# Kernel optimization log

Hardware: AMD Instinct MI355X
Metric: run time of the kernel (lower is better)

## Reference

```python
import jax, jax.numpy as jnp
import numpy as np

N_NODES = 10000
N_EDGES = 160000
F_IN, D, N_CLS = 300, 1024, 10
NEG_SLOPE = 0.2


def setup_inputs() -> dict:
    key = jax.random.key(0)
    ks = jax.random.split(key, 12)
    s = 0.05  # small init scale for numerical sanity
    return {
        "x": jax.random.normal(ks[0], (N_NODES, F_IN), jnp.float32),
        "edge_index": jax.random.randint(ks[1], (2, N_EDGES), 0, N_NODES, jnp.int64),
        "W1": jax.random.normal(ks[2], (F_IN, D), jnp.float32) * s,
        "att_src1": jax.random.normal(ks[3], (D,), jnp.float32) * s,
        "att_dst1": jax.random.normal(ks[4], (D,), jnp.float32) * s,
        "b1": jnp.zeros((D,), jnp.float32),
        "W2": jax.random.normal(ks[5], (D, D), jnp.float32) * s,
        "att_src2": jax.random.normal(ks[6], (D,), jnp.float32) * s,
        "att_dst2": jax.random.normal(ks[7], (D,), jnp.float32) * s,
        "b2": jnp.zeros((D,), jnp.float32),
        "fc_w": jax.random.normal(ks[8], (D, N_CLS), jnp.float32) * s,
        "fc_b": jnp.zeros((N_CLS,), jnp.float32),
    }


def gat_conv(x, src, dst, W, a_src, a_dst, b):
    # PyG GATConv, heads=1: h = x W; e_ij = leaky_relu(a_src.h_j + a_dst.h_i)
    h = x @ W                      # [N, D]
    e = jax.nn.leaky_relu((h @ a_src)[src] + (h @ a_dst)[dst], NEG_SLOPE)  # [E]
    # scatter-softmax over edges grouped by destination node
    m = jax.lax.stop_gradient(jax.ops.segment_max(e, dst, num_segments=N_NODES))
    ex = jnp.exp(e - m[dst])
    denom = jax.ops.segment_sum(ex, dst, num_segments=N_NODES)
    alpha = ex / denom[dst]        # [E]
    out = jax.ops.segment_sum(alpha[:, None] * h[src], dst, num_segments=N_NODES)
    return out + b


def reference(x, edge_index, W1, att_src1, att_dst1, b1,
              W2, att_src2, att_dst2, b2, fc_w, fc_b):
    loops = jnp.arange(N_NODES, dtype=edge_index.dtype)
    src = jnp.concatenate([edge_index[0], loops])  # add_self_loops=True
    dst = jnp.concatenate([edge_index[1], loops])
    emb = jax.nn.relu(gat_conv(x, src, dst, W1, att_src1, att_dst1, b1))
    emb = jax.nn.relu(gat_conv(emb, src, dst, W2, att_src2, att_dst2, b2))
    return jax.nn.softmax(emb @ fc_w + fc_b, axis=-1)
```

## Files before the change

kernel.cpp:

```cpp
#include <hip/hip_runtime.h>
#include <hip/hip_bf16.h>
#include <hip/hip_fp16.h>
#include <math.h>

#define N_NODES 10000
#define N_EDGES 160000
#define E_TOT   (N_EDGES + N_NODES)
#define F_IN    300
#define D       1024
#define N_CLS   10
#define NEG_SLOPE 0.2f

#define MP      10112
#define KP1     320
#define KP2     1024

typedef __attribute__((ext_vector_type(8))) _Float16 f16x8;
typedef __attribute__((ext_vector_type(4))) float f32x4;

#define GLOAD_LDS16(g, l) __builtin_amdgcn_global_load_lds( \
    (const __attribute__((address_space(1))) void*)(g), \
    (__attribute__((address_space(3))) void*)(l), 16, 0, 0)


__global__ void init_deg(int* __restrict__ deg) {
    int i = blockIdx.x * blockDim.x + threadIdx.x;
    if (i < N_NODES) deg[i] = 1;
}

__global__ void count_edges(const int* __restrict__ dst, int* __restrict__ deg) {
    int e = blockIdx.x * blockDim.x + threadIdx.x;
    if (e < N_EDGES) atomicAdd(&deg[dst[e]], 1);
}

__global__ void scan_offs(const int* __restrict__ deg, int* __restrict__ offs,
                          int* __restrict__ pos) {
    __shared__ int sbuf[1024];
    __shared__ int scarry;
    int t = threadIdx.x;
    if (t == 0) { scarry = 0; offs[0] = 0; }
    __syncthreads();
    for (int base = 0; base < N_NODES; base += 1024) {
        int v = (base + t < N_NODES) ? deg[base + t] : 0;
        sbuf[t] = v;
        __syncthreads();
        for (int off = 1; off < 1024; off <<= 1) {
            int add = (t >= off) ? sbuf[t - off] : 0;
            __syncthreads();
            sbuf[t] += add;
            __syncthreads();
        }
        int carry = scarry;
        if (base + t < N_NODES) {
            int incl = carry + sbuf[t];
            offs[base + t + 1] = incl;
            pos[base + t]      = incl - v;
        }
        __syncthreads();
        if (t == 1023) scarry = carry + sbuf[1023];
        __syncthreads();
    }
}

__global__ void scatter_edges(const int* __restrict__ src, const int* __restrict__ dst,
                              int* __restrict__ pos, int* __restrict__ ssrc) {
    int e = blockIdx.x * blockDim.x + threadIdx.x;
    if (e < N_EDGES) {
        int d = dst[e];
        int p = atomicAdd(&pos[d], 1);
        ssrc[p] = src[e];
    } else if (e < E_TOT) {
        int i = e - N_EDGES;
        int p = atomicAdd(&pos[i], 1);
        ssrc[p] = i;
    }
}


__global__ void prep_uv(const float* __restrict__ W1, const float* __restrict__ as1,
                        const float* __restrict__ ad1, const float* __restrict__ W2,
                        const float* __restrict__ as2, const float* __restrict__ ad2,
                        float* __restrict__ u1, float* __restrict__ v1,
                        float* __restrict__ u2, float* __restrict__ v2) {
    int wid  = (int)((blockIdx.x * blockDim.x + threadIdx.x) >> 6);
    int lane = threadIdx.x & 63;
    const float* row;
    const float* a;
    const float* b;
    float *du, *dv;
    int k;
    if (wid < F_IN) {
        k = wid; row = W1 + (size_t)k * D; a = as1; b = ad1; du = u1; dv = v1;
    } else if (wid < F_IN + D) {
        k = wid - F_IN; row = W2 + (size_t)k * D; a = as2; b = ad2; du = u2; dv = v2;
    } else return;
    float s1 = 0.f, s2 = 0.f;
    for (int n = lane; n < D; n += 64) {
        float w = row[n];
        s1 += w * a[n];
        s2 += w * b[n];
    }
    #pragma unroll
    for (int o = 32; o; o >>= 1) { s1 += __shfl_xor(s1, o); s2 += __shfl_xor(s2, o); }
    if (lane == 0) { du[k] = s1; dv[k] = s2; }
}


__global__ void node_scores_x(const float* __restrict__ x, const float* __restrict__ u1,
                              const float* __restrict__ v1, float* __restrict__ hs,
                              float* __restrict__ hd) {
    int wid  = (int)((blockIdx.x * blockDim.x + threadIdx.x) >> 6);
    int lane = threadIdx.x & 63;
    if (wid >= N_NODES) return;
    const float* row = x + (size_t)wid * F_IN;
    float s1 = 0.f, s2 = 0.f;
    for (int k = lane; k < F_IN; k += 64) {
        float v = row[k];
        s1 += v * u1[k];
        s2 += v * v1[k];
    }
    #pragma unroll
    for (int o = 32; o; o >>= 1) { s1 += __shfl_xor(s1, o); s2 += __shfl_xor(s2, o); }
    if (lane == 0) { hs[wid] = s1; hd[wid] = s2; }
}


#define ZR1 (112 * KP1)
#define ZR2 (N_NODES * 20)
#define ZR3 (112 * KP2)
#define ZTOT (2*ZR1 + 2*ZR2 + 2*ZR3 + 2*N_NODES)

__global__ void zero_misc(float* __restrict__ hs2, float* __restrict__ hd2,
                          unsigned short* __restrict__ Ah1, unsigned short* __restrict__ Al1,
                          unsigned short* __restrict__ Ah2, unsigned short* __restrict__ Al2) {
    int idx = blockIdx.x * blockDim.x + threadIdx.x;
    if (idx >= ZTOT) return;
    if (idx < 2 * ZR1) {
        unsigned short* B = (idx < ZR1) ? Ah1 : Al1;
        int off = (idx < ZR1) ? idx : idx - ZR1;
        B[(size_t)N_NODES * KP1 + off] = 0;
    } else if ((idx -= 2 * ZR1) < 2 * ZR2) {
        unsigned short* B = (idx < ZR2) ? Ah1 : Al1;
        int off = (idx < ZR2) ? idx : idx - ZR2;
        int r = off / 20, c = 300 + off % 20;
        B[(size_t)r * KP1 + c] = 0;
    } else if ((idx -= 2 * ZR2) < 2 * ZR3) {
        unsigned short* B = (idx < ZR3) ? Ah2 : Al2;
        int off = (idx < ZR3) ? idx : idx - ZR3;
        B[(size_t)N_NODES * KP2 + off] = 0;
    } else {
        idx -= 2 * ZR3;
        if (idx < N_NODES) hs2[idx] = 0.f;
        else hd2[idx - N_NODES] = 0.f;
    }
}


__global__ void transpose_f16(const float* __restrict__ W, _Float16* __restrict__ BTh,
                              int K, int N, int Kp) {
    __shared__ float tile[32][33];
    int k0 = blockIdx.x * 32, n0 = blockIdx.y * 32;
    int tx = threadIdx.x, ty = threadIdx.y;
    #pragma unroll
    for (int j = 0; j < 32; j += 8) {
        int k = k0 + ty + j;
        tile[ty + j][tx] = (k < K) ? W[(size_t)k * N + n0 + tx] : 0.f;
    }
    __syncthreads();
    #pragma unroll
    for (int j = 0; j < 32; j += 8) {
        int n = n0 + ty + j;
        int k = k0 + tx;
        BTh[(size_t)n * Kp + k] = (_Float16)tile[tx][ty + j];
    }
}


__global__ __launch_bounds__(256) void aggregate_x(
        const float* __restrict__ x, const float* __restrict__ hs,
        const float* __restrict__ hd, const int* __restrict__ offs,
        const int* __restrict__ ssrc, _Float16* __restrict__ outh,
        _Float16* __restrict__ outl) {
    int i = blockIdx.x;
    int t = threadIdx.x;
    int lane = t & 63;
    int wv = t >> 6;
    int start = offs[i], end = offs[i + 1];
    __shared__ float red[8];
    __shared__ float part[2][75][4];
    float hdi = hd[i];

    float lmax = -INFINITY;
    for (int p = start + t; p < end; p += 256) {
        float s = hs[ssrc[p]] + hdi;
        s = (s >= 0.f) ? s : s * NEG_SLOPE;
        lmax = fmaxf(lmax, s);
    }
    #pragma unroll
    for (int o = 32; o; o >>= 1) lmax = fmaxf(lmax, __shfl_xor(lmax, o));
    if (lane == 0) red[wv] = lmax;
    __syncthreads();
    float m = fmaxf(fmaxf(red[0], red[1]), fmaxf(red[2], red[3]));

    float lsum = 0.f;
    for (int p = start + t; p < end; p += 256) {
        float s = hs[ssrc[p]] + hdi;
        s = (s >= 0.f) ? s : s * NEG_SLOPE;
        lsum += __expf(s - m);
    }
    #pragma unroll
    for (int o = 32; o; o >>= 1) lsum += __shfl_xor(lsum, o);
    if (lane == 0) red[4 + wv] = lsum;
    __syncthreads();
    float inv = 1.0f / (red[4] + red[5] + red[6] + red[7]);

    int g = t / 75;
    int s = t - g * 75;
    int c = s * 4;
    float4 a = {0.f, 0.f, 0.f, 0.f};
    if (t < 225) {
        int p = start + g;
        for (; p + 3 < end; p += 6) {
            int j0 = ssrc[p], j1 = ssrc[p + 3];
            float s0 = hs[j0] + hdi; s0 = (s0 >= 0.f) ? s0 : s0 * NEG_SLOPE;
            float s1 = hs[j1] + hdi; s1 = (s1 >= 0.f) ? s1 : s1 * NEG_SLOPE;
            float w0 = __expf(s0 - m), w1 = __expf(s1 - m);
            float4 v0 = *(const float4*)(x + (size_t)j0 * F_IN + c);
            float4 v1 = *(const float4*)(x + (size_t)j1 * F_IN + c);
            a.x += w0 * v0.x + w1 * v1.x;
            a.y += w0 * v0.y + w1 * v1.y;
            a.z += w0 * v0.z + w1 * v1.z;
            a.w += w0 * v0.w + w1 * v1.w;
        }
        if (p < end) {
            int j0 = ssrc[p];
            float s0 = hs[j0] + hdi; s0 = (s0 >= 0.f) ? s0 : s0 * NEG_SLOPE;
            float w0 = __expf(s0 - m);
            float4 v0 = *(const float4*)(x + (size_t)j0 * F_IN + c);
            a.x += w0 * v0.x; a.y += w0 * v0.y; a.z += w0 * v0.z; a.w += w0 * v0.w;
        }
    }
    if (t < 225 && g > 0) {
        part[g - 1][s][0] = a.x; part[g - 1][s][1] = a.y;
        part[g - 1][s][2] = a.z; part[g - 1][s][3] = a.w;
    }
    __syncthreads();
    if (t < 75) {
        a.x += part[0][t][0] + part[1][t][0];
        a.y += part[0][t][1] + part[1][t][1];
        a.z += part[0][t][2] + part[1][t][2];
        a.w += part[0][t][3] + part[1][t][3];
        float rv[4] = {a.x * inv, a.y * inv, a.z * inv, a.w * inv};
        _Float16 hi4[4], lo4[4];
        #pragma unroll
        for (int q = 0; q < 4; ++q) {
            _Float16 hi = (_Float16)rv[q];
            hi4[q] = hi;
            lo4[q] = (_Float16)(rv[q] - (float)hi);
        }
        *(float2*)(outh + (size_t)i * KP1 + c) = *(float2*)hi4;
        *(float2*)(outl + (size_t)i * KP1 + c) = *(float2*)lo4;
    }
}


__global__ __launch_bounds__(256) void aggregate_d(
        const float* __restrict__ h, const float* __restrict__ hs,
        const float* __restrict__ hd, const int* __restrict__ offs,
        const int* __restrict__ ssrc, _Float16* __restrict__ outh,
        _Float16* __restrict__ outl) {
    int i = blockIdx.x;
    int t = threadIdx.x;
    int lane = t & 63;
    int wv = t >> 6;
    int start = offs[i], end = offs[i + 1];
    __shared__ float red[8];
    float hdi = hd[i];

    float lmax = -INFINITY;
    for (int p = start + t; p < end; p += 256) {
        float s = hs[ssrc[p]] + hdi;
        s = (s >= 0.f) ? s : s * NEG_SLOPE;
        lmax = fmaxf(lmax, s);
    }
    #pragma unroll
    for (int o = 32; o; o >>= 1) lmax = fmaxf(lmax, __shfl_xor(lmax, o));
    if (lane == 0) red[wv] = lmax;
    __syncthreads();
    float m = fmaxf(fmaxf(red[0], red[1]), fmaxf(red[2], red[3]));

    float lsum = 0.f;
    for (int p = start + t; p < end; p += 256) {
        float s = hs[ssrc[p]] + hdi;
        s = (s >= 0.f) ? s : s * NEG_SLOPE;
        lsum += __expf(s - m);
    }
    #pragma unroll
    for (int o = 32; o; o >>= 1) lsum += __shfl_xor(lsum, o);
    if (lane == 0) red[4 + wv] = lsum;
    __syncthreads();
    float inv = 1.0f / (red[4] + red[5] + red[6] + red[7]);

    int c = t * 4;
    float4 a0 = {0.f,0.f,0.f,0.f}, a1 = a0, a2 = a0, a3 = a0;
    int p = start;
    for (; p + 4 <= end; p += 4) {
        int j0 = ssrc[p], j1 = ssrc[p+1], j2 = ssrc[p+2], j3 = ssrc[p+3];
        float s0 = hs[j0] + hdi; s0 = (s0 >= 0.f) ? s0 : s0 * NEG_SLOPE;
        float s1 = hs[j1] + hdi; s1 = (s1 >= 0.f) ? s1 : s1 * NEG_SLOPE;
        float s2 = hs[j2] + hdi; s2 = (s2 >= 0.f) ? s2 : s2 * NEG_SLOPE;
        float s3 = hs[j3] + hdi; s3 = (s3 >= 0.f) ? s3 : s3 * NEG_SLOPE;
        float w0 = __expf(s0 - m), w1 = __expf(s1 - m);
        float w2 = __expf(s2 - m), w3 = __expf(s3 - m);
        float4 v0 = *(const float4*)(h + (size_t)j0 * D + c);
        float4 v1 = *(const float4*)(h + (size_t)j1 * D + c);
        float4 v2 = *(const float4*)(h + (size_t)j2 * D + c);
        float4 v3 = *(const float4*)(h + (size_t)j3 * D + c);
        a0.x += w0*v0.x; a0.y += w0*v0.y; a0.z += w0*v0.z; a0.w += w0*v0.w;
        a1.x += w1*v1.x; a1.y += w1*v1.y; a1.z += w1*v1.z; a1.w += w1*v1.w;
        a2.x += w2*v2.x; a2.y += w2*v2.y; a2.z += w2*v2.z; a2.w += w2*v2.w;
        a3.x += w3*v3.x; a3.y += w3*v3.y; a3.z += w3*v3.z; a3.w += w3*v3.w;
    }
    for (; p < end; ++p) {
        int j0 = ssrc[p];
        float s0 = hs[j0] + hdi; s0 = (s0 >= 0.f) ? s0 : s0 * NEG_SLOPE;
        float w0 = __expf(s0 - m);
        float4 v0 = *(const float4*)(h + (size_t)j0 * D + c);
        a0.x += w0*v0.x; a0.y += w0*v0.y; a0.z += w0*v0.z; a0.w += w0*v0.w;
    }
    float rv[4];
    rv[0] = ((a0.x + a1.x) + (a2.x + a3.x)) * inv;
    rv[1] = ((a0.y + a1.y) + (a2.y + a3.y)) * inv;
    rv[2] = ((a0.z + a1.z) + (a2.z + a3.z)) * inv;
    rv[3] = ((a0.w + a1.w) + (a2.w + a3.w)) * inv;
    _Float16 hi4[4], lo4[4];
    #pragma unroll
    for (int q = 0; q < 4; ++q) {
        _Float16 hi = (_Float16)rv[q];
        hi4[q] = hi;
        lo4[q] = (_Float16)(rv[q] - (float)hi);
    }
    *(float2*)(outh + (size_t)i * KP2 + c) = *(float2*)hi4;
    *(float2*)(outl + (size_t)i * KP2 + c) = *(float2*)lo4;
}


__global__ __launch_bounds__(256) void gemm_split_mfma(
        const _Float16* __restrict__ Ah, const _Float16* __restrict__ Al,
        const _Float16* __restrict__ BTh,
        float* __restrict__ C, const float* __restrict__ bias,
        const float* __restrict__ asrc, const float* __restrict__ adst,
        float* __restrict__ hs, float* __restrict__ hd,
        int Mreal, int Kp, int dots) {
    __shared__ char lds[24576];
    char* Ah_s = lds;
    char* Al_s = lds + 8192;
    char* Bh_s = lds + 16384;
    const int t    = threadIdx.x;
    const int lane = t & 63;
    const int wid  = t >> 6;
    const int chunkg = (int)gridDim.x >> 3;
    const int vid  = ((int)blockIdx.x & 7) * chunkg + ((int)blockIdx.x >> 3);
    const int n0 = (vid & 7) * 128;
    const int m0 = (vid >> 3) * 128;
    const int wr = (wid >> 1) * 64;
    const int wc = (wid & 1) * 64;
    const int fr = lane & 15;
    const int kg = lane >> 4;

    const int r0 = t >> 2, s0 = t & 3;
    const int r1 = r0 + 64;
    const int g0 = (s0 ^ ((r0 >> 1) & 3)) << 3;
    const int g1 = (s0 ^ ((r1 >> 1) & 3)) << 3;
    const size_t oA0 = (size_t)(m0 + r0) * Kp + g0;
    const size_t oA1 = (size_t)(m0 + r1) * Kp + g1;
    const size_t oB0 = (size_t)(n0 + r0) * Kp + g0;
    const size_t oB1 = (size_t)(n0 + r1) * Kp + g1;
    const int ko = (kg ^ ((fr >> 1) & 3)) << 4;

    f32x4 acc[4][4] = {};

    for (int kb = 0; kb < Kp; kb += 32) {
        GLOAD_LDS16(Ah  + oA0 + kb, Ah_s + t * 16);
        GLOAD_LDS16(Ah  + oA1 + kb, Ah_s + 4096 + t * 16);
        GLOAD_LDS16(Al  + oA0 + kb, Al_s + t * 16);
        GLOAD_LDS16(Al  + oA1 + kb, Al_s + 4096 + t * 16);
        GLOAD_LDS16(BTh + oB0 + kb, Bh_s + t * 16);
        GLOAD_LDS16(BTh + oB1 + kb, Bh_s + 4096 + t * 16);
        __syncthreads();

        f16x8 ah[4], al[4], bh[4];
        #pragma unroll
        for (int f = 0; f < 4; ++f) {
            int ra = (wr + f * 16 + fr) * 64 + ko;
            int rb = (wc + f * 16 + fr) * 64 + ko;
            ah[f] = *(const f16x8*)(Ah_s + ra);
            al[f] = *(const f16x8*)(Al_s + ra);
            bh[f] = *(const f16x8*)(Bh_s + rb);
        }
        #pragma unroll
        for (int fm = 0; fm < 4; ++fm)
            #pragma unroll
            for (int fn = 0; fn < 4; ++fn)
                acc[fm][fn] = __builtin_amdgcn_mfma_f32_16x16x32_f16(
                    ah[fm], bh[fn], acc[fm][fn], 0, 0, 0);
        #pragma unroll
        for (int fm = 0; fm < 4; ++fm)
            #pragma unroll
            for (int fn = 0; fn < 4; ++fn)
                acc[fm][fn] = __builtin_amdgcn_mfma_f32_16x16x32_f16(
                    al[fm], bh[fn], acc[fm][fn], 0, 0, 0);
        __syncthreads();
    }

    float bv[4];
    #pragma unroll
    for (int fn = 0; fn < 4; ++fn) bv[fn] = bias[n0 + wc + fn * 16 + fr];
    #pragma unroll
    for (int fm = 0; fm < 4; ++fm) {
        int mb = m0 + wr + fm * 16 + kg * 4;
        #pragma unroll
        for (int fn = 0; fn < 4; ++fn) {
            int cn = n0 + wc + fn * 16 + fr;
            #pragma unroll
            for (int j = 0; j < 4; ++j) {
                float r = fmaxf(acc[fm][fn][j] + bv[fn], 0.f);
                acc[fm][fn][j] = r;
                int m = mb + j;
                if (m < Mreal) C[(size_t)m * 1024 + cn] = r;
            }
        }
    }

    if (dots) {
        float av[4], dv[4];
        #pragma unroll
        for (int fn = 0; fn < 4; ++fn) {
            int cn = n0 + wc + fn * 16 + fr;
            av[fn] = asrc[cn];
            dv[fn] = adst[cn];
        }
        #pragma unroll
        for (int fm = 0; fm < 4; ++fm) {
            #pragma unroll
            for (int j = 0; j < 4; ++j) {
                float v1 = acc[fm][0][j] * av[0] + acc[fm][1][j] * av[1]
                         + acc[fm][2][j] * av[2] + acc[fm][3][j] * av[3];
                float v2 = acc[fm][0][j] * dv[0] + acc[fm][1][j] * dv[1]
                         + acc[fm][2][j] * dv[2] + acc[fm][3][j] * dv[3];
                #pragma unroll
                for (int o = 1; o < 16; o <<= 1) {
                    v1 += __shfl_xor(v1, o);
                    v2 += __shfl_xor(v2, o);
                }
                int m = m0 + wr + fm * 16 + kg * 4 + j;
                if (fr == 0 && m < Mreal) {
                    atomicAdd(&hs[m], v1);
                    atomicAdd(&hd[m], v2);
                }
            }
        }
    }
}


__global__ void fc_softmax(const float* __restrict__ emb, const float* __restrict__ fcw,
                           const float* __restrict__ fcb, float* __restrict__ out) {
    int wid  = (int)((blockIdx.x * blockDim.x + threadIdx.x) >> 6);
    int lane = threadIdx.x & 63;
    if (wid >= N_NODES) return;
    float acc[N_CLS] = {};
    const float* row = emb + (size_t)wid * D;
    for (int k = lane * 4; k < D; k += 256) {
        float4 v = *(const float4*)(row + k);
        #pragma unroll
        for (int c = 0; c < N_CLS; ++c)
            acc[c] += v.x * fcw[k * N_CLS + c] + v.y * fcw[(k+1) * N_CLS + c]
                    + v.z * fcw[(k+2) * N_CLS + c] + v.w * fcw[(k+3) * N_CLS + c];
    }
    #pragma unroll
    for (int c = 0; c < N_CLS; ++c) {
        #pragma unroll
        for (int o = 32; o; o >>= 1) acc[c] += __shfl_xor(acc[c], o);
    }
    if (lane == 0) {
        float logit[N_CLS];
        float m = -INFINITY;
        #pragma unroll
        for (int c = 0; c < N_CLS; ++c) { logit[c] = acc[c] + fcb[c]; m = fmaxf(m, logit[c]); }
        float s = 0.f;
        #pragma unroll
        for (int c = 0; c < N_CLS; ++c) { logit[c] = __expf(logit[c] - m); s += logit[c]; }
        float invs = 1.0f / s;
        #pragma unroll
        for (int c = 0; c < N_CLS; ++c) out[(size_t)wid * N_CLS + c] = logit[c] * invs;
    }
}


extern "C" void kernel_launch(void* const* d_in, const int* in_sizes, int n_in,
                              void* d_out, int out_size, void* d_ws, size_t ws_size,
                              hipStream_t stream) {
    const float* x        = (const float*)d_in[0];
    const int*   ei       = (const int*)d_in[1];
    const float* W1       = (const float*)d_in[2];
    const float* att_src1 = (const float*)d_in[3];
    const float* att_dst1 = (const float*)d_in[4];
    const float* b1       = (const float*)d_in[5];
    const float* W2       = (const float*)d_in[6];
    const float* att_src2 = (const float*)d_in[7];
    const float* att_dst2 = (const float*)d_in[8];
    const float* b2       = (const float*)d_in[9];
    const float* fc_w     = (const float*)d_in[10];
    const float* fc_b     = (const float*)d_in[11];
    float* out = (float*)d_out;

    const int* src = ei;
    const int* dst = ei + N_EDGES;

    char* w = (char*)d_ws;
    #define ALLOC(name, bytes) char* name = w; w += (((size_t)(bytes) + 255) & ~(size_t)255)
    ALLOC(p_emb,   (size_t)N_NODES * D * 4);
    ALLOC(p_hs1,   (size_t)N_NODES * 4);
    ALLOC(p_hd1,   (size_t)N_NODES * 4);
    ALLOC(p_hs2,   (size_t)N_NODES * 4);
    ALLOC(p_hd2,   (size_t)N_NODES * 4);
    ALLOC(p_deg,   (size_t)N_NODES * 4);
    ALLOC(p_offs,  (size_t)(N_NODES + 1) * 4);
    ALLOC(p_pos,   (size_t)N_NODES * 4);
    ALLOC(p_ssrc,  (size_t)E_TOT * 4);
    ALLOC(p_u1,    (size_t)F_IN * 4);
    ALLOC(p_v1,    (size_t)F_IN * 4);
    ALLOC(p_u2,    (size_t)D * 4);
    ALLOC(p_v2,    (size_t)D * 4);
    ALLOC(p_as1,   (size_t)2 * MP * KP1 * 2);
    ALLOC(p_as2,   (size_t)2 * MP * KP2 * 2);
    ALLOC(p_bt1,   (size_t)D * KP1 * 2);
    ALLOC(p_bt2,   (size_t)D * KP2 * 2);
    #undef ALLOC

    float* emb  = (float*)p_emb;
    float* hs1  = (float*)p_hs1;
    float* hd1  = (float*)p_hd1;
    float* hs2  = (float*)p_hs2;
    float* hd2  = (float*)p_hd2;
    int*   deg  = (int*)p_deg;
    int*   offs = (int*)p_offs;
    int*   pos  = (int*)p_pos;
    int*   ssrc = (int*)p_ssrc;
    float* u1 = (float*)p_u1; float* v1 = (float*)p_v1;
    float* u2 = (float*)p_u2; float* v2 = (float*)p_v2;
    _Float16* Ah1  = (_Float16*)p_as1;
    _Float16* Al1  = Ah1 + (size_t)MP * KP1;
    _Float16* Ah2  = (_Float16*)p_as2;
    _Float16* Al2  = Ah2 + (size_t)MP * KP2;
    _Float16* BT1h = (_Float16*)p_bt1;
    _Float16* BT2h = (_Float16*)p_bt2;

    init_deg<<<(N_NODES + 255) / 256, 256, 0, stream>>>(deg);
    count_edges<<<(N_EDGES + 255) / 256, 256, 0, stream>>>(dst, deg);
    scan_offs<<<1, 1024, 0, stream>>>(deg, offs, pos);
    scatter_edges<<<(E_TOT + 255) / 256, 256, 0, stream>>>(src, dst, pos, ssrc);

    prep_uv<<<((F_IN + D) * 64 + 255) / 256, 256, 0, stream>>>(
        W1, att_src1, att_dst1, W2, att_src2, att_dst2, u1, v1, u2, v2);
    dim3 tb(32, 8);
    transpose_f16<<<dim3(KP1 / 32, D / 32), tb, 0, stream>>>(W1, BT1h, F_IN, D, KP1);
    transpose_f16<<<dim3(KP2 / 32, D / 32), tb, 0, stream>>>(W2, BT2h, D, D, KP2);
    zero_misc<<<(ZTOT + 255) / 256, 256, 0, stream>>>(hs2, hd2,
        (unsigned short*)Ah1, (unsigned short*)Al1,
        (unsigned short*)Ah2, (unsigned short*)Al2);

    const int gemmGrid = (D / 128) * (MP / 128);

    node_scores_x<<<(N_NODES * 64 + 255) / 256, 256, 0, stream>>>(x, u1, v1, hs1, hd1);
    aggregate_x<<<N_NODES, 256, 0, stream>>>(x, hs1, hd1, offs, ssrc, Ah1, Al1);
    gemm_split_mfma<<<gemmGrid, 256, 0, stream>>>(Ah1, Al1, BT1h, emb, b1,
                                                  u2, v2, hs2, hd2, N_NODES, KP1, 1);

    aggregate_d<<<N_NODES, 256, 0, stream>>>(emb, hs2, hd2, offs, ssrc, Ah2, Al2);
    gemm_split_mfma<<<gemmGrid, 256, 0, stream>>>(Ah2, Al2, BT2h, emb, b2,
                                                  (const float*)nullptr, (const float*)nullptr,
                                                  (float*)nullptr, (float*)nullptr,
                                                  N_NODES, KP2, 0);

    fc_softmax<<<(N_NODES * 64 + 255) / 256, 256, 0, stream>>>(emb, fc_w, fc_b, out);
}
```

Before: 381.5 us.

## Store layer-1 embedding in fp16 for gather and double-buffer GEMM LDS stages

The first GEMM now writes its ReLU output as fp16 instead of fp32, and the second-layer aggregation gathers fp16 rows and accumulates in fp32. This halves the bytes moved by the memory-bound edge gather. Separately, the MFMA GEMM gets two LDS buffers so the next K-slice is loaded while the current one is computed, which removes one barrier per iteration. The cost is double the LDS footprint, which may lower occupancy, and precision loss from rounding the intermediate embedding to fp16.

```diff
diff --git a/kernel.cpp b/kernel.cpp
--- a/kernel.cpp
+++ b/kernel.cpp
@@ -16,6 +16,7 @@
 #define KP2     1024
 
 typedef __attribute__((ext_vector_type(8))) _Float16 f16x8;
+typedef __attribute__((ext_vector_type(4))) _Float16 f16x4;
 typedef __attribute__((ext_vector_type(4))) float f32x4;
 
 #define GLOAD_LDS16(g, l) __builtin_amdgcn_global_load_lds( \
@@ -265,7 +266,7 @@
 
 
 __global__ __launch_bounds__(256) void aggregate_d(
-        const float* __restrict__ h, const float* __restrict__ hs,
+        const _Float16* __restrict__ h, const float* __restrict__ hs,
         const float* __restrict__ hd, const int* __restrict__ offs,
         const int* __restrict__ ssrc, _Float16* __restrict__ outh,
         _Float16* __restrict__ outl) {
@@ -312,21 +313,21 @@
         float s3 = hs[j3] + hdi; s3 = (s3 >= 0.f) ? s3 : s3 * NEG_SLOPE;
         float w0 = __expf(s0 - m), w1 = __expf(s1 - m);
         float w2 = __expf(s2 - m), w3 = __expf(s3 - m);
-        float4 v0 = *(const float4*)(h + (size_t)j0 * D + c);
-        float4 v1 = *(const float4*)(h + (size_t)j1 * D + c);
-        float4 v2 = *(const float4*)(h + (size_t)j2 * D + c);
-        float4 v3 = *(const float4*)(h + (size_t)j3 * D + c);
-        a0.x += w0*v0.x; a0.y += w0*v0.y; a0.z += w0*v0.z; a0.w += w0*v0.w;
-        a1.x += w1*v1.x; a1.y += w1*v1.y; a1.z += w1*v1.z; a1.w += w1*v1.w;
-        a2.x += w2*v2.x; a2.y += w2*v2.y; a2.z += w2*v2.z; a2.w += w2*v2.w;
-        a3.x += w3*v3.x; a3.y += w3*v3.y; a3.z += w3*v3.z; a3.w += w3*v3.w;
+        f16x4 v0 = *(const f16x4*)(h + (size_t)j0 * D + c);
+        f16x4 v1 = *(const f16x4*)(h + (size_t)j1 * D + c);
+        f16x4 v2 = *(const f16x4*)(h + (size_t)j2 * D + c);
+        f16x4 v3 = *(const f16x4*)(h + (size_t)j3 * D + c);
+        a0.x += w0*(float)v0.x; a0.y += w0*(float)v0.y; a0.z += w0*(float)v0.z; a0.w += w0*(float)v0.w;
+        a1.x += w1*(float)v1.x; a1.y += w1*(float)v1.y; a1.z += w1*(float)v1.z; a1.w += w1*(float)v1.w;
+        a2.x += w2*(float)v2.x; a2.y += w2*(float)v2.y; a2.z += w2*(float)v2.z; a2.w += w2*(float)v2.w;
+        a3.x += w3*(float)v3.x; a3.y += w3*(float)v3.y; a3.z += w3*(float)v3.z; a3.w += w3*(float)v3.w;
     }
     for (; p < end; ++p) {
         int j0 = ssrc[p];
         float s0 = hs[j0] + hdi; s0 = (s0 >= 0.f) ? s0 : s0 * NEG_SLOPE;
         float w0 = __expf(s0 - m);
-        float4 v0 = *(const float4*)(h + (size_t)j0 * D + c);
-        a0.x += w0*v0.x; a0.y += w0*v0.y; a0.z += w0*v0.z; a0.w += w0*v0.w;
+        f16x4 v0 = *(const f16x4*)(h + (size_t)j0 * D + c);
+        a0.x += w0*(float)v0.x; a0.y += w0*(float)v0.y; a0.z += w0*(float)v0.z; a0.w += w0*(float)v0.w;
     }
     float rv[4];
     rv[0] = ((a0.x + a1.x) + (a2.x + a3.x)) * inv;
@@ -348,14 +349,12 @@
 __global__ __launch_bounds__(256) void gemm_split_mfma(
         const _Float16* __restrict__ Ah, const _Float16* __restrict__ Al,
         const _Float16* __restrict__ BTh,
-        float* __restrict__ C, const float* __restrict__ bias,
+        float* __restrict__ Cf, _Float16* __restrict__ Ch,
+        const float* __restrict__ bias,
         const float* __restrict__ asrc, const float* __restrict__ adst,
         float* __restrict__ hs, float* __restrict__ hd,
         int Mreal, int Kp, int dots) {
-    __shared__ char lds[24576];
-    char* Ah_s = lds;
-    char* Al_s = lds + 8192;
-    char* Bh_s = lds + 16384;
+    __shared__ char lds[49152];
     const int t    = threadIdx.x;
     const int lane = t & 63;
     const int wid  = t >> 6;
@@ -380,23 +379,31 @@
 
     f32x4 acc[4][4] = {};
 
+    auto STAGE = [&](int b, int kb) {
+        char* base = lds + b * 24576;
+        GLOAD_LDS16(Ah  + oA0 + kb, base + t * 16);
+        GLOAD_LDS16(Ah  + oA1 + kb, base + 4096  + t * 16);
+        GLOAD_LDS16(Al  + oA0 + kb, base + 8192  + t * 16);
+        GLOAD_LDS16(Al  + oA1 + kb, base + 12288 + t * 16);
+        GLOAD_LDS16(BTh + oB0 + kb, base + 16384 + t * 16);
+        GLOAD_LDS16(BTh + oB1 + kb, base + 20480 + t * 16);
+    };
+
+    STAGE(0, 0);
+    __syncthreads();
+
+    int cur = 0;
     for (int kb = 0; kb < Kp; kb += 32) {
-        GLOAD_LDS16(Ah  + oA0 + kb, Ah_s + t * 16);
-        GLOAD_LDS16(Ah  + oA1 + kb, Ah_s + 4096 + t * 16);
-        GLOAD_LDS16(Al  + oA0 + kb, Al_s + t * 16);
-        GLOAD_LDS16(Al  + oA1 + kb, Al_s + 4096 + t * 16);
-        GLOAD_LDS16(BTh + oB0 + kb, Bh_s + t * 16);
-        GLOAD_LDS16(BTh + oB1 + kb, Bh_s + 4096 + t * 16);
-        __syncthreads();
-
+        if (kb + 32 < Kp) STAGE(cur ^ 1, kb + 32);
+        char* base = lds + cur * 24576;
         f16x8 ah[4], al[4], bh[4];
         #pragma unroll
         for (int f = 0; f < 4; ++f) {
             int ra = (wr + f * 16 + fr) * 64 + ko;
             int rb = (wc + f * 16 + fr) * 64 + ko;
-            ah[f] = *(const f16x8*)(Ah_s + ra);
-            al[f] = *(const f16x8*)(Al_s + ra);
-            bh[f] = *(const f16x8*)(Bh_s + rb);
+            ah[f] = *(const f16x8*)(base + ra);
+            al[f] = *(const f16x8*)(base + 8192 + ra);
+            bh[f] = *(const f16x8*)(base + 16384 + rb);
         }
         #pragma unroll
         for (int fm = 0; fm < 4; ++fm)
@@ -411,6 +418,7 @@
                 acc[fm][fn] = __builtin_amdgcn_mfma_f32_16x16x32_f16(
                     al[fm], bh[fn], acc[fm][fn], 0, 0, 0);
         __syncthreads();
+        cur ^= 1;
     }
 
     float bv[4];
@@ -427,7 +435,10 @@
                 float r = fmaxf(acc[fm][fn][j] + bv[fn], 0.f);
                 acc[fm][fn][j] = r;
                 int m = mb + j;
-                if (m < Mreal) C[(size_t)m * 1024 + cn] = r;
+                if (m < Mreal) {
+                    if (Cf) Cf[(size_t)m * 1024 + cn] = r;
+                    else    Ch[(size_t)m * 1024 + cn] = (_Float16)r;
+                }
             }
         }
     }
@@ -521,6 +532,7 @@
     char* w = (char*)d_ws;
     #define ALLOC(name, bytes) char* name = w; w += (((size_t)(bytes) + 255) & ~(size_t)255)
     ALLOC(p_emb,   (size_t)N_NODES * D * 4);
+    ALLOC(p_embh,  (size_t)N_NODES * D * 2);
     ALLOC(p_hs1,   (size_t)N_NODES * 4);
     ALLOC(p_hd1,   (size_t)N_NODES * 4);
     ALLOC(p_hs2,   (size_t)N_NODES * 4);
@@ -540,6 +552,7 @@
     #undef ALLOC
 
     float* emb  = (float*)p_emb;
+    _Float16* embh = (_Float16*)p_embh;
     float* hs1  = (float*)p_hs1;
     float* hd1  = (float*)p_hd1;
     float* hs2  = (float*)p_hs2;
@@ -575,11 +588,13 @@
 
     node_scores_x<<<(N_NODES * 64 + 255) / 256, 256, 0, stream>>>(x, u1, v1, hs1, hd1);
     aggregate_x<<<N_NODES, 256, 0, stream>>>(x, hs1, hd1, offs, ssrc, Ah1, Al1);
-    gemm_split_mfma<<<gemmGrid, 256, 0, stream>>>(Ah1, Al1, BT1h, emb, b1,
+    gemm_split_mfma<<<gemmGrid, 256, 0, stream>>>(Ah1, Al1, BT1h,
+                                                  (float*)nullptr, embh, b1,
                                                   u2, v2, hs2, hd2, N_NODES, KP1, 1);
 
-    aggregate_d<<<N_NODES, 256, 0, stream>>>(emb, hs2, hd2, offs, ssrc, Ah2, Al2);
-    gemm_split_mfma<<<gemmGrid, 256, 0, stream>>>(Ah2, Al2, BT2h, emb, b2,
+    aggregate_d<<<N_NODES, 256, 0, stream>>>(embh, hs2, hd2, offs, ssrc, Ah2, Al2);
+    gemm_split_mfma<<<gemmGrid, 256, 0, stream>>>(Ah2, Al2, BT2h,
+                                                  emb, (_Float16*)nullptr, b2,
                                                   (const float*)nullptr, (const float*)nullptr,
                                                   (float*)nullptr, (float*)nullptr,
                                                   N_NODES, KP2, 0);
```

New measurement: 338.4 us. -11.3%, faster.
